# Optimization experiments

Measured on AMD Instinct MI355X. Metric: run time of the kernel, lower is better.

Reference implementation:

```python
import jax, jax.numpy as jnp
import numpy as np

B, TQ, TK, D, H = 2, 2048, 2048, 1024, 16


def setup_inputs() -> dict:
    key = jax.random.key(0)
    ks = jax.random.split(key, 8)
    s = 1.0 / np.sqrt(D)
    x_q = jax.random.normal(ks[0], (B, TQ, D), jnp.float32)
    x_k = jax.random.normal(ks[1], (B, TK, D), jnp.float32)
    x_v = jax.random.normal(ks[2], (B, TK, D), jnp.float32)
    # causal mask, True = masked (matches masked_fill semantics)
    causal = jnp.triu(jnp.ones((TQ, TK), jnp.bool_), k=1)
    attn_mask = jnp.broadcast_to(causal, (B, TQ, TK))
    Wq = jax.random.normal(ks[3], (D, D), jnp.float32) * s
    Wk = jax.random.normal(ks[4], (D, D), jnp.float32) * s
    Wv = jax.random.normal(ks[5], (D, D), jnp.float32) * s
    Wo = jax.random.normal(ks[6], (D, D), jnp.float32) * s
    z = jnp.zeros((D,), jnp.float32)
    return {"x_q": x_q, "x_k": x_k, "x_v": x_v, "attn_mask": attn_mask,
            "Wq": Wq, "bq": z, "Wk": Wk, "bk": z, "Wv": Wv, "bv": z,
            "Wo": Wo, "bo": z, "n_heads": H}


def reference(x_q, x_k, x_v, attn_mask, Wq, bq, Wk, bk, Wv, bv, Wo, bo, n_heads):
    Bv, Tq, Dm = x_q.shape
    Tk = x_k.shape[1]
    dh = Dm // n_heads
    # nn.Linear: y = x @ W^T + b; split heads -> [B, H, T, dh]
    Q = (jnp.einsum('btd,od->bto', x_q, Wq) + bq).reshape(Bv, Tq, n_heads, dh).transpose(0, 2, 1, 3)
    K = (jnp.einsum('btd,od->bto', x_k, Wk) + bk).reshape(Bv, Tk, n_heads, dh).transpose(0, 2, 1, 3)
    V = (jnp.einsum('btd,od->bto', x_v, Wv) + bv).reshape(Bv, Tk, n_heads, dh).transpose(0, 2, 1, 3)
    scale = 1.0 / np.sqrt(dh).astype(np.float32)
    scores = jnp.einsum('bhqd,bhkd->bhqk', Q, K) * scale  # [B,H,Tq,Tk]
    scores = jnp.where(attn_mask[:, None, :, :], -jnp.inf, scores)
    A = jax.nn.softmax(scores, axis=-1)  # dropout p=0.0 -> identity
    out = jnp.einsum('bhqk,bhkd->bhqd', A, V)
    out = out.transpose(0, 2, 1, 3).reshape(Bv, Tq, Dm)
    return jnp.einsum('btd,od->bto', out, Wo) + bo
```

## Files before the change

### kernel.cpp

```cpp
#include <hip/hip_runtime.h>


typedef __attribute__((ext_vector_type(8))) __bf16 bf16x8;
typedef __attribute__((ext_vector_type(4))) float f32x4;
typedef unsigned short u16;

constexpr int BATCH  = 2;
constexpr int TSEQ   = 2048;
constexpr int DMODEL = 1024;
constexpr int NHEAD  = 16;
constexpr int DHEAD  = 64;
constexpr int MROWS  = BATCH * TSEQ;

static __device__ __forceinline__ u16 f2bf(float f) {
  union { float f; unsigned int u; } v; v.f = f;
  unsigned int u = v.u;
  return (u16)((u + 0x7fffu + ((u >> 16) & 1u)) >> 16);
}

static __device__ __forceinline__ void gload16(const void* g, void* l) {
  __builtin_amdgcn_global_load_lds(
      (const __attribute__((address_space(1))) void*)g,
      (__attribute__((address_space(3))) void*)l, 16, 0, 0);
}

__global__ __launch_bounds__(256) void cvt_multi(const float* __restrict__ s0,
                                                 const float* __restrict__ s1,
                                                 const float* __restrict__ s2,
                                                 const float* __restrict__ s3,
                                                 u16* __restrict__ d0, u16* __restrict__ d1,
                                                 u16* __restrict__ d2, u16* __restrict__ d3,
                                                 int n4) {
  const float* s; u16* d;
  switch (blockIdx.y) {
    case 0: s = s0; d = d0; break;
    case 1: s = s1; d = d1; break;
    case 2: s = s2; d = d2; break;
    default: s = s3; d = d3; break;
  }
  int i = blockIdx.x * 256 + threadIdx.x;
  if (i >= n4) return;
  float4 f = ((const float4*)s)[i];
  ushort4 o;
  o.x = f2bf(f.x); o.y = f2bf(f.y); o.z = f2bf(f.z); o.w = f2bf(f.w);
  ((ushort4*)d)[i] = o;
}

template <typename Epi>
static __device__ __forceinline__ void gemm_body(const u16* __restrict__ X_,
                                                 const u16* __restrict__ W_,
                                                 const float* __restrict__ bias,
                                                 Epi epi) {
  __shared__ __align__(16) u16 As[2][4096];
  __shared__ __align__(16) u16 Bs[2][4096];
  const int lane = threadIdx.x & 63, wave = threadIdx.x >> 6;
  const int l16 = lane & 15, lk = lane >> 4;
  const int wm = wave >> 2, wn = wave & 3;
  const int row0 = blockIdx.x * 128, col0 = blockIdx.y * 128;
  constexpr int K = DMODEL;
  const u16* ga = X_ + (size_t)(row0 + wave * 16 + l16) * K + lk * 8;
  const u16* gb = W_ + (size_t)(col0 + wave * 16 + l16) * K + lk * 8;
  f32x4 acc[4][2];
#pragma unroll
  for (int mt = 0; mt < 4; ++mt)
#pragma unroll
    for (int nt = 0; nt < 2; ++nt) acc[mt][nt] = (f32x4){0.f, 0.f, 0.f, 0.f};
  gload16(ga, &As[0][wave * 512]);
  gload16(gb, &Bs[0][wave * 512]);
  __syncthreads();
  int buf = 0;
  for (int ks = 0; ks < K / 32; ++ks) {
    if (ks + 1 < K / 32) {
      gload16(ga + (ks + 1) * 32, &As[buf ^ 1][wave * 512]);
      gload16(gb + (ks + 1) * 32, &Bs[buf ^ 1][wave * 512]);
    }
    bf16x8 a[4], b[2];
#pragma unroll
    for (int mt = 0; mt < 4; ++mt)
      a[mt] = *(const bf16x8*)&As[buf][(wm * 4 + mt) * 512 + lane * 8];
#pragma unroll
    for (int nt = 0; nt < 2; ++nt)
      b[nt] = *(const bf16x8*)&Bs[buf][(wn * 2 + nt) * 512 + lane * 8];
#pragma unroll
    for (int mt = 0; mt < 4; ++mt)
#pragma unroll
      for (int nt = 0; nt < 2; ++nt)
        acc[mt][nt] =
            __builtin_amdgcn_mfma_f32_16x16x32_bf16(a[mt], b[nt], acc[mt][nt], 0, 0, 0);
    __syncthreads();
    buf ^= 1;
  }
#pragma unroll
  for (int mt = 0; mt < 4; ++mt)
#pragma unroll
    for (int nt = 0; nt < 2; ++nt)
#pragma unroll
      for (int r = 0; r < 4; ++r) {
        int m = row0 + wm * 64 + mt * 16 + lk * 4 + r;
        int n = col0 + wn * 32 + nt * 16 + l16;
        float v = acc[mt][nt][r] + bias[n];
        epi(m, n, v);
      }
}

__global__ __launch_bounds__(512) void gemm_qkv(
    const u16* __restrict__ xq, const u16* __restrict__ xk, const u16* __restrict__ xv,
    const u16* __restrict__ wq, const u16* __restrict__ wk, const u16* __restrict__ wv,
    const float* __restrict__ bq, const float* __restrict__ bk, const float* __restrict__ bv,
    u16* __restrict__ Qh, u16* __restrict__ Kh, u16* __restrict__ Vt) {
  const int z = blockIdx.z;
  const u16* X = z == 0 ? xq : (z == 1 ? xk : xv);
  const u16* W = z == 0 ? wq : (z == 1 ? wk : wv);
  const float* bias = z == 0 ? bq : (z == 1 ? bk : bv);
  u16* O01 = z == 0 ? Qh : Kh;
  gemm_body(X, W, bias, [&](int m, int n, float v) {
    int bb = m >> 11, t = m & (TSEQ - 1);
    int h = n >> 6, dd = n & (DHEAD - 1);
    if (z == 2)
      Vt[(((size_t)(bb * NHEAD + h)) * DHEAD + dd) * TSEQ + t] = f2bf(v);
    else
      O01[(((size_t)(bb * NHEAD + h)) * TSEQ + t) * DHEAD + dd] = f2bf(v);
  });
}

__global__ __launch_bounds__(512) void gemm_o(const u16* __restrict__ AO,
                                              const u16* __restrict__ wo,
                                              const float* __restrict__ bias,
                                              float* __restrict__ out) {
  gemm_body(AO, wo, bias,
            [&](int m, int n, float v) { out[(size_t)m * DMODEL + n] = v; });
}

__global__ __launch_bounds__(256) void flash_attn(const u16* __restrict__ Qh,
                                                  const u16* __restrict__ Kh,
                                                  const u16* __restrict__ Vt,
                                                  u16* __restrict__ AO) {
  const int lane = threadIdx.x & 63, wave = threadIdx.x >> 6;
  const int l16 = lane & 15, lk = lane >> 4;
  const int bh = blockIdx.x;
  const int qt = (gridDim.y - 1) - blockIdx.y;
  const int q0 = qt * 64;
  const int b = bh >> 4, h = bh & 15;

  __shared__ __align__(16) u16 Kl[2][4096];
  __shared__ __align__(16) u16 Vl[2][4096];
  __shared__ __align__(16) u16 plds[4][16][72];

  const u16* Qb = Qh + (size_t)bh * TSEQ * DHEAD;
  const u16* Kb = Kh + (size_t)bh * TSEQ * DHEAD;
  const u16* Vb = Vt + (size_t)bh * DHEAD * TSEQ;

  bf16x8 qf[2];
  {
    const u16* qp = Qb + (size_t)(q0 + wave * 16 + l16) * DHEAD + lk * 8;
    qf[0] = *(const bf16x8*)(qp);
    qf[1] = *(const bf16x8*)(qp + 32);
  }

  float mrow[4], lrow[4];
  f32x4 acco[4];
#pragma unroll
  for (int r = 0; r < 4; ++r) { mrow[r] = -1e30f; lrow[r] = 0.f; }
#pragma unroll
  for (int dt = 0; dt < 4; ++dt) acco[dt] = (f32x4){0.f, 0.f, 0.f, 0.f};

  auto stage_kv = [&](int bufi, int kbase) {
#pragma unroll
    for (int j = 0; j < 2; ++j) {
      int s = j * 4 + wave;
      int trow = (s >> 1) * 16 + l16;
      int dhs = (s & 1) * 4 + lk;
      gload16(Kb + (size_t)(kbase + trow) * DHEAD + dhs * 8, &Kl[bufi][s * 512]);
      gload16(Vb + (size_t)trow * TSEQ + kbase + dhs * 8, &Vl[bufi][s * 512]);
    }
  };

  const int nkb = qt + 1;
  stage_kv(0, 0);
  __syncthreads();
  int buf = 0;
  const int qrow_base = q0 + wave * 16 + 4 * lk;

  for (int kb = 0; kb < nkb; ++kb) {
    const int kbase = kb * 64;
    if (kb + 1 < nkb) stage_kv(buf ^ 1, kbase + 64);

    f32x4 s[4];
#pragma unroll
    for (int nt = 0; nt < 4; ++nt) {
      bf16x8 k0f = *(const bf16x8*)&Kl[buf][nt * 1024 + lane * 8];
      bf16x8 k1f = *(const bf16x8*)&Kl[buf][nt * 1024 + 512 + lane * 8];
      f32x4 z = (f32x4){0.f, 0.f, 0.f, 0.f};
      z = __builtin_amdgcn_mfma_f32_16x16x32_bf16(qf[0], k0f, z, 0, 0, 0);
      z = __builtin_amdgcn_mfma_f32_16x16x32_bf16(qf[1], k1f, z, 0, 0, 0);
      s[nt] = z;
    }
#pragma unroll
    for (int r = 0; r < 4; ++r) {
      const int qrow = qrow_base + r;
      float mx = -1e30f;
#pragma unroll
      for (int nt = 0; nt < 4; ++nt) {
        float v = s[nt][r] * 0.125f;
        int kcol = kbase + nt * 16 + l16;
        v = (kcol <= qrow) ? v : -1e30f;
        s[nt][r] = v;
        mx = fmaxf(mx, v);
      }
#pragma unroll
      for (int off = 1; off < 16; off <<= 1) mx = fmaxf(mx, __shfl_xor(mx, off, 16));
      float mnew = fmaxf(mrow[r], mx);
      float alpha = __expf(mrow[r] - mnew);
      float rs = 0.f;
#pragma unroll
      for (int nt = 0; nt < 4; ++nt) {
        float p = __expf(s[nt][r] - mnew);
        s[nt][r] = p;
        rs += p;
      }
#pragma unroll
      for (int off = 1; off < 16; off <<= 1) rs += __shfl_xor(rs, off, 16);
      lrow[r] = lrow[r] * alpha + rs;
      mrow[r] = mnew;
#pragma unroll
      for (int dt = 0; dt < 4; ++dt) acco[dt][r] *= alpha;
    }
#pragma unroll
    for (int nt = 0; nt < 4; ++nt)
#pragma unroll
      for (int r = 0; r < 4; ++r)
        plds[wave][4 * lk + r][nt * 16 + l16] = f2bf(s[nt][r]);
    bf16x8 pf0 = *(const bf16x8*)&plds[wave][l16][lk * 8];
    bf16x8 pf1 = *(const bf16x8*)&plds[wave][l16][32 + lk * 8];
#pragma unroll
    for (int dt = 0; dt < 4; ++dt) {
      bf16x8 v0 = *(const bf16x8*)&Vl[buf][dt * 1024 + lane * 8];
      bf16x8 v1 = *(const bf16x8*)&Vl[buf][dt * 1024 + 512 + lane * 8];
      acco[dt] = __builtin_amdgcn_mfma_f32_16x16x32_bf16(pf0, v0, acco[dt], 0, 0, 0);
      acco[dt] = __builtin_amdgcn_mfma_f32_16x16x32_bf16(pf1, v1, acco[dt], 0, 0, 0);
    }
    __syncthreads();
    buf ^= 1;
  }

#pragma unroll
  for (int dt = 0; dt < 4; ++dt)
#pragma unroll
    for (int r = 0; r < 4; ++r) {
      int t = qrow_base + r;
      int col = h * DHEAD + dt * 16 + l16;
      float v = acco[dt][r] / lrow[r];
      AO[((size_t)(b * TSEQ + t)) * DMODEL + col] = f2bf(v);
    }
}

extern "C" void kernel_launch(void* const* d_in, const int* in_sizes, int n_in,
                              void* d_out, int out_size, void* d_ws, size_t ws_size,
                              hipStream_t stream) {
  const float* x_q = (const float*)d_in[0];
  const float* x_k = (const float*)d_in[1];
  const float* x_v = (const float*)d_in[2];
  const float* Wq = (const float*)d_in[4];
  const float* bq = (const float*)d_in[5];
  const float* Wk = (const float*)d_in[6];
  const float* bk = (const float*)d_in[7];
  const float* Wv = (const float*)d_in[8];
  const float* bv = (const float*)d_in[9];
  const float* Wo = (const float*)d_in[10];
  const float* bo = (const float*)d_in[11];

  const size_t nx = (size_t)MROWS * DMODEL;
  const size_t nw = (size_t)DMODEL * DMODEL;
  u16* ws   = (u16*)d_ws;
  u16* xq_b = ws;
  u16* xk_b = xq_b + nx;
  u16* xv_b = xk_b + nx;
  u16* wq_b = xv_b + nx;
  u16* wk_b = wq_b + nw;
  u16* wv_b = wk_b + nw;
  u16* wo_b = wv_b + nw;
  u16* Qh   = wo_b + nw;
  u16* Kh   = Qh + nx;
  u16* Vt   = Kh + nx;
  u16* AO   = Vt + nx;

  const int n4x = (int)(nx / 4), n4w = (int)(nw / 4);
  cvt_multi<<<dim3((n4x + 255) / 256, 3), 256, 0, stream>>>(
      x_q, x_k, x_v, nullptr, xq_b, xk_b, xv_b, nullptr, n4x);
  cvt_multi<<<dim3((n4w + 255) / 256, 4), 256, 0, stream>>>(
      Wq, Wk, Wv, Wo, wq_b, wk_b, wv_b, wo_b, n4w);

  gemm_qkv<<<dim3(MROWS / 128, DMODEL / 128, 3), 512, 0, stream>>>(
      xq_b, xk_b, xv_b, wq_b, wk_b, wv_b, bq, bk, bv, Qh, Kh, Vt);

  flash_attn<<<dim3(BATCH * NHEAD, TSEQ / 64), 256, 0, stream>>>(Qh, Kh, Vt, AO);

  gemm_o<<<dim3(MROWS / 128, DMODEL / 128), 512, 0, stream>>>(AO, wo_b, bo, (float*)d_out);
}
```

Baseline: 175.9 us.

## Enlarge attention q-tile to 128 with 8 waves, lazy rescale, fold scale into Q

The flash attention kernel now handles 128 query rows per block with 8 waves sharing each staged K/V tile, which halves the K/V global traffic per query row. Waves skip key tiles beyond their own diagonal, and the causal mask is applied only on the diagonal tile. The online softmax rescales only when the new row max exceeds the running max by more than a threshold, and the lane-level row sum is reduced once at the end. The 1/sqrt(dh) scale is folded into the Q projection epilogue. The trade-offs are idle waves in the upper-half tiles, fewer blocks in the grid, and a lazy rescale that lets exponentials reach up to e^8 before correction.

```diff
diff --git a/kernel.cpp b/kernel.cpp
--- a/kernel.cpp
+++ b/kernel.cpp
@@ -116,6 +116,7 @@
   gemm_body(X, W, bias, [&](int m, int n, float v) {
     int bb = m >> 11, t = m & (TSEQ - 1);
     int h = n >> 6, dd = n & (DHEAD - 1);
+    if (z == 0) v *= 0.125f;
     if (z == 2)
       Vt[(((size_t)(bb * NHEAD + h)) * DHEAD + dd) * TSEQ + t] = f2bf(v);
     else
@@ -131,20 +132,20 @@
             [&](int m, int n, float v) { out[(size_t)m * DMODEL + n] = v; });
 }
 
-__global__ __launch_bounds__(256) void flash_attn(const u16* __restrict__ Qh,
-                                                  const u16* __restrict__ Kh,
-                                                  const u16* __restrict__ Vt,
-                                                  u16* __restrict__ AO) {
+__global__ __launch_bounds__(512, 6) void flash_attn(const u16* __restrict__ Qh,
+                                                     const u16* __restrict__ Kh,
+                                                     const u16* __restrict__ Vt,
+                                                     u16* __restrict__ AO) {
   const int lane = threadIdx.x & 63, wave = threadIdx.x >> 6;
   const int l16 = lane & 15, lk = lane >> 4;
   const int bh = blockIdx.x;
   const int qt = (gridDim.y - 1) - blockIdx.y;
-  const int q0 = qt * 64;
+  const int q0 = qt * 128;
   const int b = bh >> 4, h = bh & 15;
 
   __shared__ __align__(16) u16 Kl[2][4096];
   __shared__ __align__(16) u16 Vl[2][4096];
-  __shared__ __align__(16) u16 plds[4][16][72];
+  __shared__ __align__(16) u16 plds[8][16][72];
 
   const u16* Qb = Qh + (size_t)bh * TSEQ * DHEAD;
   const u16* Kb = Kh + (size_t)bh * TSEQ * DHEAD;
@@ -157,25 +158,22 @@
     qf[1] = *(const bf16x8*)(qp + 32);
   }
 
-  float mrow[4], lrow[4];
+  float mrow[4], lsum[4];
   f32x4 acco[4];
 #pragma unroll
-  for (int r = 0; r < 4; ++r) { mrow[r] = -1e30f; lrow[r] = 0.f; }
+  for (int r = 0; r < 4; ++r) { mrow[r] = -1e30f; lsum[r] = 0.f; }
 #pragma unroll
   for (int dt = 0; dt < 4; ++dt) acco[dt] = (f32x4){0.f, 0.f, 0.f, 0.f};
 
   auto stage_kv = [&](int bufi, int kbase) {
-#pragma unroll
-    for (int j = 0; j < 2; ++j) {
-      int s = j * 4 + wave;
-      int trow = (s >> 1) * 16 + l16;
-      int dhs = (s & 1) * 4 + lk;
-      gload16(Kb + (size_t)(kbase + trow) * DHEAD + dhs * 8, &Kl[bufi][s * 512]);
-      gload16(Vb + (size_t)trow * TSEQ + kbase + dhs * 8, &Vl[bufi][s * 512]);
-    }
+    int trow = (wave >> 1) * 16 + l16;
+    int dhs = (wave & 1) * 4 + lk;
+    gload16(Kb + (size_t)(kbase + trow) * DHEAD + dhs * 8, &Kl[bufi][wave * 512]);
+    gload16(Vb + (size_t)trow * TSEQ + kbase + dhs * 8, &Vl[bufi][wave * 512]);
   };
 
-  const int nkb = qt + 1;
+  const int nkb = 2 * qt + 2;
+  const int kbdiag = 2 * qt + (wave >> 2);
   stage_kv(0, 0);
   __syncthreads();
   int buf = 0;
@@ -185,72 +183,88 @@
     const int kbase = kb * 64;
     if (kb + 1 < nkb) stage_kv(buf ^ 1, kbase + 64);
 
-    f32x4 s[4];
-#pragma unroll
-    for (int nt = 0; nt < 4; ++nt) {
-      bf16x8 k0f = *(const bf16x8*)&Kl[buf][nt * 1024 + lane * 8];
-      bf16x8 k1f = *(const bf16x8*)&Kl[buf][nt * 1024 + 512 + lane * 8];
-      f32x4 z = (f32x4){0.f, 0.f, 0.f, 0.f};
-      z = __builtin_amdgcn_mfma_f32_16x16x32_bf16(qf[0], k0f, z, 0, 0, 0);
-      z = __builtin_amdgcn_mfma_f32_16x16x32_bf16(qf[1], k1f, z, 0, 0, 0);
-      s[nt] = z;
-    }
-#pragma unroll
-    for (int r = 0; r < 4; ++r) {
-      const int qrow = qrow_base + r;
-      float mx = -1e30f;
+    if (kb <= kbdiag) {
+      f32x4 s[4];
 #pragma unroll
       for (int nt = 0; nt < 4; ++nt) {
-        float v = s[nt][r] * 0.125f;
-        int kcol = kbase + nt * 16 + l16;
-        v = (kcol <= qrow) ? v : -1e30f;
-        s[nt][r] = v;
-        mx = fmaxf(mx, v);
-      }
-#pragma unroll
-      for (int off = 1; off < 16; off <<= 1) mx = fmaxf(mx, __shfl_xor(mx, off, 16));
-      float mnew = fmaxf(mrow[r], mx);
-      float alpha = __expf(mrow[r] - mnew);
-      float rs = 0.f;
-#pragma unroll
-      for (int nt = 0; nt < 4; ++nt) {
-        float p = __expf(s[nt][r] - mnew);
-        s[nt][r] = p;
-        rs += p;
-      }
-#pragma unroll
-      for (int off = 1; off < 16; off <<= 1) rs += __shfl_xor(rs, off, 16);
-      lrow[r] = lrow[r] * alpha + rs;
-      mrow[r] = mnew;
-#pragma unroll
-      for (int dt = 0; dt < 4; ++dt) acco[dt][r] *= alpha;
-    }
-#pragma unroll
-    for (int nt = 0; nt < 4; ++nt)
+        bf16x8 k0f = *(const bf16x8*)&Kl[buf][nt * 1024 + lane * 8];
+        bf16x8 k1f = *(const bf16x8*)&Kl[buf][nt * 1024 + 512 + lane * 8];
+        f32x4 z = (f32x4){0.f, 0.f, 0.f, 0.f};
+        z = __builtin_amdgcn_mfma_f32_16x16x32_bf16(qf[0], k0f, z, 0, 0, 0);
+        z = __builtin_amdgcn_mfma_f32_16x16x32_bf16(qf[1], k1f, z, 0, 0, 0);
+        s[nt] = z;
+      }
+      if (kb == kbdiag) {
+#pragma unroll
+        for (int nt = 0; nt < 4; ++nt)
+#pragma unroll
+          for (int r = 0; r < 4; ++r) {
+            int kcol = kbase + nt * 16 + l16;
+            s[nt][r] = (kcol <= qrow_base + r) ? s[nt][r] : -1e30f;
+          }
+      }
+      float pmax[4];
+      bool need = false;
+#pragma unroll
+      for (int r = 0; r < 4; ++r) {
+        pmax[r] = fmaxf(fmaxf(s[0][r], s[1][r]), fmaxf(s[2][r], s[3][r]));
+        need |= (pmax[r] > mrow[r] + 8.f);
+      }
+      if (__any(need)) {
+#pragma unroll
+        for (int r = 0; r < 4; ++r) {
+          float mx = pmax[r];
+#pragma unroll
+          for (int off = 1; off < 16; off <<= 1) mx = fmaxf(mx, __shfl_xor(mx, off, 16));
+          float mnew = fmaxf(mrow[r], mx);
+          float alpha = __expf(mrow[r] - mnew);
+          lsum[r] *= alpha;
+#pragma unroll
+          for (int dt = 0; dt < 4; ++dt) acco[dt][r] *= alpha;
+          mrow[r] = mnew;
+        }
+      }
 #pragma unroll
       for (int r = 0; r < 4; ++r)
-        plds[wave][4 * lk + r][nt * 16 + l16] = f2bf(s[nt][r]);
-    bf16x8 pf0 = *(const bf16x8*)&plds[wave][l16][lk * 8];
-    bf16x8 pf1 = *(const bf16x8*)&plds[wave][l16][32 + lk * 8];
-#pragma unroll
-    for (int dt = 0; dt < 4; ++dt) {
-      bf16x8 v0 = *(const bf16x8*)&Vl[buf][dt * 1024 + lane * 8];
-      bf16x8 v1 = *(const bf16x8*)&Vl[buf][dt * 1024 + 512 + lane * 8];
-      acco[dt] = __builtin_amdgcn_mfma_f32_16x16x32_bf16(pf0, v0, acco[dt], 0, 0, 0);
-      acco[dt] = __builtin_amdgcn_mfma_f32_16x16x32_bf16(pf1, v1, acco[dt], 0, 0, 0);
+#pragma unroll
+        for (int nt = 0; nt < 4; ++nt) {
+          float p = __expf(s[nt][r] - mrow[r]);
+          s[nt][r] = p;
+          lsum[r] += p;
+        }
+#pragma unroll
+      for (int nt = 0; nt < 4; ++nt)
+#pragma unroll
+        for (int r = 0; r < 4; ++r)
+          plds[wave][4 * lk + r][nt * 16 + l16] = f2bf(s[nt][r]);
+      bf16x8 pf0 = *(const bf16x8*)&plds[wave][l16][lk * 8];
+      bf16x8 pf1 = *(const bf16x8*)&plds[wave][l16][32 + lk * 8];
+#pragma unroll
+      for (int dt = 0; dt < 4; ++dt) {
+        bf16x8 v0 = *(const bf16x8*)&Vl[buf][dt * 1024 + lane * 8];
+        bf16x8 v1 = *(const bf16x8*)&Vl[buf][dt * 1024 + 512 + lane * 8];
+        acco[dt] = __builtin_amdgcn_mfma_f32_16x16x32_bf16(pf0, v0, acco[dt], 0, 0, 0);
+        acco[dt] = __builtin_amdgcn_mfma_f32_16x16x32_bf16(pf1, v1, acco[dt], 0, 0, 0);
+      }
     }
     __syncthreads();
     buf ^= 1;
   }
 
 #pragma unroll
+  for (int r = 0; r < 4; ++r) {
+    float t = lsum[r];
+#pragma unroll
+    for (int off = 1; off < 16; off <<= 1) t += __shfl_xor(t, off, 16);
+    lsum[r] = 1.f / t;
+  }
+#pragma unroll
   for (int dt = 0; dt < 4; ++dt)
 #pragma unroll
     for (int r = 0; r < 4; ++r) {
       int t = qrow_base + r;
       int col = h * DHEAD + dt * 16 + l16;
-      float v = acco[dt][r] / lrow[r];
-      AO[((size_t)(b * TSEQ + t)) * DMODEL + col] = f2bf(v);
+      AO[((size_t)(b * TSEQ + t)) * DMODEL + col] = f2bf(acco[dt][r] * lsum[r]);
     }
 }
 
@@ -293,7 +307,7 @@
   gemm_qkv<<<dim3(MROWS / 128, DMODEL / 128, 3), 512, 0, stream>>>(
       xq_b, xk_b, xv_b, wq_b, wk_b, wv_b, bq, bk, bv, Qh, Kh, Vt);
 
-  flash_attn<<<dim3(BATCH * NHEAD, TSEQ / 64), 256, 0, stream>>>(Qh, Kh, Vt, AO);
+  flash_attn<<<dim3(BATCH * NHEAD, TSEQ / 128), 512, 0, stream>>>(Qh, Kh, Vt, AO);
 
   gemm_o<<<dim3(MROWS / 128, DMODEL / 128), 512, 0, stream>>>(AO, wo_b, bo, (float*)d_out);
 }
```

After: 158.2 us. -10.1%, faster.
